# Optimization experiments

Measured on AMD Instinct MI355X. Metric: run time of the kernel, lower is better.

The kernel has to match this reference:

```python
import jax, jax.numpy as jnp
import numpy as np

B, S, D = 2, 2048, 768
H = 12
HD = D // H  # 64
SCALE = HD ** -0.5


def setup_inputs() -> dict:
    key = jax.random.key(0)
    k1, k2, k3, k4, k5 = jax.random.split(key, 5)
    x = jax.random.normal(k1, (B, S, D), dtype=jnp.float32)
    w_qkv = jax.random.normal(k2, (D, 3 * D), dtype=jnp.float32) * (D ** -0.5)
    b_qkv = jax.random.normal(k3, (3 * D,), dtype=jnp.float32) * 0.02
    w_proj = jax.random.normal(k4, (D, D), dtype=jnp.float32) * (D ** -0.5)
    b_proj = jax.random.normal(k5, (D,), dtype=jnp.float32) * 0.02
    return {"x": x, "w_qkv": w_qkv, "b_qkv": b_qkv, "w_proj": w_proj, "b_proj": b_proj}


def reference(x, w_qkv, b_qkv, w_proj, b_proj):
    b, s, d = x.shape
    # QKV projection: (B,S,3D) -> (3,B,H,S,HD)
    qkv = x @ w_qkv + b_qkv
    qkv = qkv.reshape(b, s, 3, H, HD).transpose(2, 0, 3, 1, 4)
    q, k, v = qkv[0], qkv[1], qkv[2]
    q = q * SCALE
    # full NxN attention scores, as in the original module
    attn = jnp.einsum("bhqd,bhkd->bhqk", q, k)
    attn = jax.nn.softmax(attn, axis=-1)
    out = jnp.einsum("bhqk,bhkd->bhqd", attn, v)  # (B,H,S,HD)
    out = out.transpose(0, 2, 1, 3).reshape(b, s, d)
    return out @ w_proj + b_proj
```

## Files before the change

kernel.cpp:

```cpp
#include <hip/hip_runtime.h>
#include <hip/hip_bf16.h>

#define B_ 2
#define S_ 2048
#define D_ 768
#define H_ 12
#define HD_ 64
#define EXP2C_ 0.1803368801111244f

typedef __attribute__((ext_vector_type(8))) short bf16x8;
typedef __attribute__((ext_vector_type(8))) unsigned short u16x8;
typedef __attribute__((ext_vector_type(4))) float f32x4;
typedef __attribute__((ext_vector_type(4))) unsigned int u32x4;

static __device__ __forceinline__ unsigned short f2bf(float x) {
    union { float f; unsigned u; } v; v.f = x;
    unsigned r = (v.u + 0x7FFFu + ((v.u >> 16) & 1u)) >> 16;
    return (unsigned short)r;
}
static __device__ __forceinline__ float bf2f(unsigned short h) {
    union { unsigned u; float f; } v; v.u = ((unsigned)h) << 16;
    return v.f;
}
static __device__ __forceinline__ float fexp2(float x) { return __builtin_exp2f(x); }

static __device__ __forceinline__ unsigned pk_bf16(float a, float b) {
    __hip_bfloat162 pk = __float22bfloat162_rn(make_float2(a, b));
    union { __hip_bfloat162 h; unsigned u; } v; v.h = pk;
    return v.u;
}

static __device__ __forceinline__ f32x4 mfma32(bf16x8 a, bf16x8 b, f32x4 c) {
    return __builtin_amdgcn_mfma_f32_16x16x32_bf16(a, b, c, 0, 0, 0);
}

typedef __attribute__((address_space(3))) unsigned int lds_u32;
typedef __attribute__((address_space(1))) const unsigned int glb_u32;
static __device__ __forceinline__ void glds16(const unsigned short* g, unsigned short* l) {
    __builtin_amdgcn_global_load_lds((glb_u32*)g, (lds_u32*)l, 16, 0, 0);
}

#define PREP_CONV_ 1536
#define PREP_TQKV_ 1728
#define PREP_TPRJ_ 576
__global__ __launch_bounds__(256) void prep_kernel(
    const float* __restrict__ x,      unsigned short* __restrict__ x16,
    const float* __restrict__ w_qkv,  unsigned short* __restrict__ wqkvT,
    const float* __restrict__ w_proj, unsigned short* __restrict__ wprojT)
{
    __shared__ float tile[32][33];
    const int bid = blockIdx.x, t = threadIdx.x;
    if (bid < PREP_CONV_) {
        const int i = (bid * 256 + t) * 8;
        float4 a0 = *(const float4*)(x + i);
        float4 a1 = *(const float4*)(x + i + 4);
        u16x8 s;
        s[0] = f2bf(a0.x); s[1] = f2bf(a0.y); s[2] = f2bf(a0.z); s[3] = f2bf(a0.w);
        s[4] = f2bf(a1.x); s[5] = f2bf(a1.y); s[6] = f2bf(a1.z); s[7] = f2bf(a1.w);
        *(u16x8*)(x16 + i) = s;
        return;
    }
    const float* w; unsigned short* wT; int N, bb;
    if (bid < PREP_CONV_ + PREP_TQKV_) { w = w_qkv; wT = wqkvT; N = 3 * D_; bb = bid - PREP_CONV_; }
    else                               { w = w_proj; wT = wprojT; N = D_;   bb = bid - PREP_CONV_ - PREP_TQKV_; }
    const int K = D_;
    const int nt = N / 32;
    const int n0 = (bb % nt) * 32, k0 = (bb / nt) * 32;
    const int tx = t & 31, ty = t >> 5;
#pragma unroll
    for (int i = 0; i < 4; i++)
        tile[ty + i * 8][tx] = w[(size_t)(k0 + ty + i * 8) * N + n0 + tx];
    __syncthreads();
#pragma unroll
    for (int i = 0; i < 4; i++)
        wT[(size_t)(n0 + ty + i * 8) * K + k0 + tx] = f2bf(tile[tx][ty + i * 8]);
}

template <int BM, int BN, bool OUT_F32>
__global__ __launch_bounds__(256) void gemm_bt_kernel(
    const unsigned short* __restrict__ A,
    const unsigned short* __restrict__ Bt,
    const float* __restrict__ bias,
    void* __restrict__ Cp,
    int M, int N, int K)
{
    constexpr int BK = 64;
    __shared__ __align__(16) unsigned short As[BM][BK];
    __shared__ __align__(16) unsigned short Bs[BN][BK];
    constexpr int MI = BM / 32, NJ = BN / 32;
    constexpr int ACH = BM * BK / 8;
    constexpr int BCH = BN * BK / 8;

    const int t = threadIdx.x;
    const int w = t >> 6, lane = t & 63, quad = lane >> 4, l16 = lane & 15;
    const int n0 = blockIdx.x * BN, m0 = blockIdx.y * BM;
    const int mw = (w & 1) * (BM / 2), nw = (w >> 1) * (BN / 2);

    const f32x4 z = {0.f, 0.f, 0.f, 0.f};
    f32x4 acc[MI][NJ];
#pragma unroll
    for (int i = 0; i < MI; i++)
#pragma unroll
        for (int j = 0; j < NJ; j++) acc[i][j] = z;

    for (int kk = 0; kk < K; kk += BK) {
#pragma unroll
        for (int it = 0; it < ACH / 256; it++) {
            const int c = t + it * 256;
            const int row = c >> 3, gs = (c & 7) ^ (row & 7);
            glds16(A + (size_t)(m0 + row) * K + kk + gs * 8, &As[0][0] + c * 8);
        }
#pragma unroll
        for (int it = 0; it < BCH / 256; it++) {
            const int c = t + it * 256;
            const int row = c >> 3, gs = (c & 7) ^ (row & 7);
            glds16(Bt + (size_t)(n0 + row) * K + kk + gs * 8, &Bs[0][0] + c * 8);
        }
        __syncthreads();

#pragma unroll
        for (int k2 = 0; k2 < 2; k2++) {
            bf16x8 a[MI], b[NJ];
#pragma unroll
            for (int i = 0; i < MI; i++) {
                const int row = mw + i * 16 + l16;
                const int p = (quad + k2 * 4) ^ (row & 7);
                a[i] = *(const bf16x8*)(&As[row][p * 8]);
            }
#pragma unroll
            for (int j = 0; j < NJ; j++) {
                const int row = nw + j * 16 + l16;
                const int p = (quad + k2 * 4) ^ (row & 7);
                b[j] = *(const bf16x8*)(&Bs[row][p * 8]);
            }
#pragma unroll
            for (int i = 0; i < MI; i++)
#pragma unroll
                for (int j = 0; j < NJ; j++)
                    acc[i][j] = mfma32(a[i], b[j], acc[i][j]);
        }
        __syncthreads();
    }

#pragma unroll
    for (int j = 0; j < NJ; j++) {
        const int col = n0 + nw + j * 16 + l16;
        const float bv = bias[col];
#pragma unroll
        for (int i = 0; i < MI; i++) {
#pragma unroll
            for (int r = 0; r < 4; r++) {
                const int row = m0 + mw + i * 16 + quad * 4 + r;
                const float v = acc[i][j][r] + bv;
                if (OUT_F32) ((float*)Cp)[(size_t)row * N + col] = v;
                else         ((unsigned short*)Cp)[(size_t)row * N + col] = f2bf(v);
            }
        }
    }
}

__global__ __launch_bounds__(256) void repack_v_kernel(
    const unsigned short* __restrict__ qkv,
    unsigned short* __restrict__ vt)
{
    __shared__ unsigned short T[64][65];
    const int t = threadIdx.x;
    const int bh = blockIdx.x, st = blockIdx.y;
    const int b = bh / H_, h = bh % H_;
    const unsigned short* src =
        qkv + (size_t)(b * S_ + st * 64) * (3 * D_) + 2 * D_ + h * HD_;

#pragma unroll
    for (int it = 0; it < 2; it++) {
        const int c = t + it * 256, sr = c >> 3, g = c & 7;
        u16x8 v = *(const u16x8*)(src + (size_t)sr * (3 * D_) + g * 8);
#pragma unroll
        for (int j = 0; j < 8; j++) T[sr][g * 8 + j] = v[j];
    }
    __syncthreads();
#pragma unroll
    for (int it = 0; it < 2; it++) {
        const int c = t + it * 256, hd = c >> 3, g = c & 7;
        u16x8 v;
#pragma unroll
        for (int j = 0; j < 8; j++) v[j] = T[g * 8 + j][hd];
        *(u16x8*)(vt + (size_t)(bh * HD_ + hd) * S_ + st * 64 + g * 8) = v;
    }
}

__global__ __launch_bounds__(256) void attn_kernel(
    const unsigned short* __restrict__ qkv,
    const unsigned short* __restrict__ vt,
    float* __restrict__ o_p0,
    float* __restrict__ o_p1,
    float* __restrict__ l_p)
{
    __shared__ __align__(16) unsigned short Ks[2][64][64];
    __shared__ __align__(16) unsigned short Vs[2][64][64];

    const int t = threadIdx.x;
    const int w = t >> 6, lane = t & 63, quad = lane >> 4, l16 = lane & 15;
    const int h8 = l16 & 7;
    const int qt = blockIdx.x, bh = blockIdx.y, ks = blockIdx.z;
    const int b = bh / H_, h = bh % H_;
    const int ld = 3 * D_;

    const unsigned short* qbase =
        qkv + (size_t)(b * S_ + qt * 64 + 16 * w + l16) * ld + h * HD_;
    u16x8 qr0 = *(const u16x8*)(qbase + quad * 8);
    u16x8 qr1 = *(const u16x8*)(qbase + 32 + quad * 8);
    bf16x8 qf0, qf1;
#pragma unroll
    for (int j = 0; j < 8; j++) {
        qf0[j] = (short)f2bf(bf2f(qr0[j]) * EXP2C_);
        qf1[j] = (short)f2bf(bf2f(qr1[j]) * EXP2C_);
    }

    bf16x8 ones;
#pragma unroll
    for (int j = 0; j < 8; j++) ones[j] = (short)0x3F80;

    const unsigned short* kbase =
        qkv + (size_t)(b * S_ + ks * 1024) * ld + D_ + h * HD_;
    const unsigned short* vbase = vt + (size_t)bh * HD_ * S_;

    const int c0 = t, c1 = t + 256;
    const int row0 = c0 >> 3, row1 = c1 >> 3;
    const int kg0 = (c0 & 7) ^ ((row0 & 3) | (((row0 >> 3) & 1) << 2));
    const int kg1 = (c1 & 7) ^ ((row1 & 3) | (((row1 >> 3) & 1) << 2));
    const int vg0 = (c0 & 7) ^ (row0 & 7);
    const int vg1 = (c1 & 7) ^ (row1 & 7);
    const unsigned short* kp0 = kbase + (size_t)row0 * ld + kg0 * 8;
    const unsigned short* kp1 = kbase + (size_t)row1 * ld + kg1 * 8;
    const unsigned short* vp0 = vbase + (size_t)row0 * S_ + ks * 1024 + vg0 * 8;
    const unsigned short* vp1 = vbase + (size_t)row1 * S_ + ks * 1024 + vg1 * 8;
    const size_t KSTEP = (size_t)64 * ld;

    const f32x4 z = {0.f, 0.f, 0.f, 0.f};
    f32x4 o_acc[4] = {z, z, z, z};
    f32x4 l_acc = z;

    glds16(kp0, &Ks[0][0][0] + c0 * 8);
    glds16(kp1, &Ks[0][0][0] + c1 * 8);
    glds16(vp0, &Vs[0][0][0] + c0 * 8);
    glds16(vp1, &Vs[0][0][0] + c1 * 8);
    kp0 += KSTEP; kp1 += KSTEP; vp0 += 64; vp1 += 64;
    __syncthreads();

    const int NT = 1024 / 64;
    for (int kt = 0; kt < NT; kt++) {
        const int buf = kt & 1;

        if (kt + 1 < NT) {
            unsigned short* kd = &Ks[buf ^ 1][0][0];
            unsigned short* vd = &Vs[buf ^ 1][0][0];
            glds16(kp0, kd + c0 * 8);
            glds16(kp1, kd + c1 * 8);
            glds16(vp0, vd + c0 * 8);
            glds16(vp1, vd + c1 * 8);
            kp0 += KSTEP; kp1 += KSTEP; vp0 += 64; vp1 += 64;
        }

        f32x4 s_acc[4] = {z, z, z, z};
        __builtin_amdgcn_s_setprio(1);
#pragma unroll
        for (int nt = 0; nt < 4; nt++) {
            const int rowp = ((nt >> 1) << 5) + ((l16 >> 2) << 3) + ((nt & 1) << 2) + (l16 & 3);
            const int skr = (rowp & 3) | (((rowp >> 3) & 1) << 2);
            const unsigned short* kr = &Ks[buf][rowp][0];
            bf16x8 k0 = *(const bf16x8*)(kr + (quad ^ skr) * 8);
            bf16x8 k1 = *(const bf16x8*)(kr + ((quad ^ skr) ^ 4) * 8);
            s_acc[nt] = mfma32(k0, qf0, s_acc[nt]);
            s_acc[nt] = mfma32(k1, qf1, s_acc[nt]);
        }
        __builtin_amdgcn_s_setprio(0);

        bf16x8 vr0[4], vr1[4];
#pragma unroll
        for (int nt = 0; nt < 4; nt++) {
            const int row = nt * 16 + l16;
            vr0[nt] = *(const bf16x8*)(&Vs[buf][row][(quad ^ h8) * 8]);
            vr1[nt] = *(const bf16x8*)(&Vs[buf][row][((quad ^ h8) ^ 4) * 8]);
        }

        f32x4 pr[4];
#pragma unroll
        for (int nt = 0; nt < 4; nt++) {
#pragma unroll
            for (int r = 0; r < 4; r++) pr[nt][r] = fexp2(s_acc[nt][r]);
        }
        union { u32x4 u; bf16x8 h; } ca, cb;
        ca.u[0] = pk_bf16(pr[0][0], pr[0][1]);
        ca.u[1] = pk_bf16(pr[0][2], pr[0][3]);
        ca.u[2] = pk_bf16(pr[1][0], pr[1][1]);
        ca.u[3] = pk_bf16(pr[1][2], pr[1][3]);
        cb.u[0] = pk_bf16(pr[2][0], pr[2][1]);
        cb.u[1] = pk_bf16(pr[2][2], pr[2][3]);
        cb.u[2] = pk_bf16(pr[3][0], pr[3][1]);
        cb.u[3] = pk_bf16(pr[3][2], pr[3][3]);
        const bf16x8 pa0 = ca.h, pa1 = cb.h;

        __builtin_amdgcn_s_setprio(1);
        l_acc = mfma32(pa0, ones, l_acc);
        l_acc = mfma32(pa1, ones, l_acc);
#pragma unroll
        for (int nt = 0; nt < 4; nt++) {
            o_acc[nt] = mfma32(pa0, vr0[nt], o_acc[nt]);
            o_acc[nt] = mfma32(pa1, vr1[nt], o_acc[nt]);
        }
        __builtin_amdgcn_s_setprio(0);

        __syncthreads();
    }

    float* op = ks ? o_p1 : o_p0;
    float* lp2 = l_p + (size_t)ks * (B_ * S_ * H_);
#pragma unroll
    for (int r = 0; r < 4; r++) {
        const int row = b * S_ + qt * 64 + 16 * w + quad * 4 + r;
        float* ob = op + (size_t)row * D_ + h * HD_;
#pragma unroll
        for (int nt = 0; nt < 4; nt++)
            ob[nt * 16 + l16] = o_acc[nt][r];
        if (l16 == 0) lp2[(size_t)row * H_ + h] = l_acc[r];
    }
}

__global__ __launch_bounds__(256) void combine_kernel(
    const float* __restrict__ o_p0,
    const float* __restrict__ o_p1,
    const float* __restrict__ l_p,
    unsigned short* __restrict__ o)
{
    const int i = (blockIdx.x * 256 + threadIdx.x) * 8;
    const int row = i / D_, col = i - row * D_, h = col >> 6;
    const float l0 = l_p[(size_t)row * H_ + h];
    const float l1 = l_p[(size_t)(B_ * S_ * H_) + row * H_ + h];
    const float inv = 1.f / (l0 + l1);
    float4 a0 = *(const float4*)(o_p0 + i);
    float4 a1 = *(const float4*)(o_p0 + i + 4);
    float4 b0 = *(const float4*)(o_p1 + i);
    float4 b1 = *(const float4*)(o_p1 + i + 4);
    u16x8 s;
    s[0] = f2bf((a0.x + b0.x) * inv); s[1] = f2bf((a0.y + b0.y) * inv);
    s[2] = f2bf((a0.z + b0.z) * inv); s[3] = f2bf((a0.w + b0.w) * inv);
    s[4] = f2bf((a1.x + b1.x) * inv); s[5] = f2bf((a1.y + b1.y) * inv);
    s[6] = f2bf((a1.z + b1.z) * inv); s[7] = f2bf((a1.w + b1.w) * inv);
    *(u16x8*)(o + i) = s;
}

extern "C" void kernel_launch(void* const* d_in, const int* in_sizes, int n_in,
                              void* d_out, int out_size, void* d_ws, size_t ws_size,
                              hipStream_t stream) {
    const float* x      = (const float*)d_in[0];
    const float* w_qkv  = (const float*)d_in[1];
    const float* b_qkv  = (const float*)d_in[2];
    const float* w_proj = (const float*)d_in[3];
    const float* b_proj = (const float*)d_in[4];
    float* out = (float*)d_out;

    unsigned short* qkv    = (unsigned short*)d_ws;
    unsigned short* vtb    = qkv    + (size_t)(B_ * S_) * (3 * D_);
    unsigned short* o_x16  = vtb    + (size_t)(B_ * H_) * HD_ * S_;
    unsigned short* wqkvT  = o_x16  + (size_t)(B_ * S_) * D_;
    unsigned short* wprojT = wqkvT  + (size_t)D_ * (3 * D_);
    float* o_p1 = (float*)(wprojT + (size_t)D_ * D_);
    float* l_p  = o_p1 + (size_t)(B_ * S_) * D_;
    float* o_p0 = out;

    dim3 blk(256);
    prep_kernel<<<dim3(PREP_CONV_ + PREP_TQKV_ + PREP_TPRJ_), blk, 0, stream>>>(
        x, o_x16, w_qkv, wqkvT, w_proj, wprojT);
    gemm_bt_kernel<128, 96, false><<<dim3((3 * D_) / 96, (B_ * S_) / 128), blk, 0, stream>>>(
        o_x16, wqkvT, b_qkv, qkv, B_ * S_, 3 * D_, D_);
    repack_v_kernel<<<dim3(B_ * H_, S_ / 64), blk, 0, stream>>>(qkv, vtb);
    attn_kernel<<<dim3(S_ / 64, B_ * H_, 2), blk, 0, stream>>>(qkv, vtb, o_p0, o_p1, l_p);
    combine_kernel<<<dim3((B_ * S_) * D_ / (256 * 8)), blk, 0, stream>>>(
        o_p0, o_p1, l_p, o_x16);
    gemm_bt_kernel<64, 64, true><<<dim3(D_ / 64, (B_ * S_) / 64), blk, 0, stream>>>(
        o_x16, wprojT, b_proj, out, B_ * S_, D_, D_);
}
```

Before: 171.2 us.

## Fuse V transpose into QKV GEMM epilogue and remap attention grid per XCD

The QKV GEMM epilogue now writes the V columns directly in transposed per-head layout, so the separate repack_v kernel and its extra read and write of V are no longer needed. The attention launch becomes a 1D grid whose block index is remapped so that all query tiles of one (head, split) group land on the same XCD, aiming for better L2 reuse of K/V. The s_setprio hints around the MFMA sections are also removed. The transposed V store writes 8-byte chunks with a large stride, which may coalesce poorly, and the block remapping assumes a fixed count of 8 XCDs.

```diff
diff --git a/kernel.cpp b/kernel.cpp
--- a/kernel.cpp
+++ b/kernel.cpp
@@ -76,12 +76,13 @@
         wT[(size_t)(n0 + ty + i * 8) * K + k0 + tx] = f2bf(tile[tx][ty + i * 8]);
 }
 
-template <int BM, int BN, bool OUT_F32>
+template <int BM, int BN, bool OUT_F32, bool VSPLIT>
 __global__ __launch_bounds__(256) void gemm_bt_kernel(
     const unsigned short* __restrict__ A,
     const unsigned short* __restrict__ Bt,
     const float* __restrict__ bias,
     void* __restrict__ Cp,
+    unsigned short* __restrict__ vt,
     int M, int N, int K)
 {
     constexpr int BK = 64;
@@ -142,6 +143,28 @@
         __syncthreads();
     }
 
+    if (VSPLIT && n0 >= 2 * D_) {
+#pragma unroll
+        for (int j = 0; j < NJ; j++) {
+            const int gcol = n0 + nw + j * 16 + l16;
+            const int col = gcol - 2 * D_;
+            const int hh = col >> 6, hd = col & 63;
+            const float bv = bias[gcol];
+#pragma unroll
+            for (int i = 0; i < MI; i++) {
+                const int row = m0 + mw + i * 16 + quad * 4;
+                const int bb = row >> 11, ss = row & 2047;
+                unsigned long long pkv = 0;
+#pragma unroll
+                for (int r = 0; r < 4; r++)
+                    pkv |= (unsigned long long)f2bf(acc[i][j][r] + bv) << (16 * r);
+                *(unsigned long long*)(vt +
+                    ((size_t)(bb * H_ + hh) * HD_ + hd) * S_ + ss) = pkv;
+            }
+        }
+        return;
+    }
+
 #pragma unroll
     for (int j = 0; j < NJ; j++) {
         const int col = n0 + nw + j * 16 + l16;
@@ -156,35 +179,6 @@
                 else         ((unsigned short*)Cp)[(size_t)row * N + col] = f2bf(v);
             }
         }
-    }
-}
-
-__global__ __launch_bounds__(256) void repack_v_kernel(
-    const unsigned short* __restrict__ qkv,
-    unsigned short* __restrict__ vt)
-{
-    __shared__ unsigned short T[64][65];
-    const int t = threadIdx.x;
-    const int bh = blockIdx.x, st = blockIdx.y;
-    const int b = bh / H_, h = bh % H_;
-    const unsigned short* src =
-        qkv + (size_t)(b * S_ + st * 64) * (3 * D_) + 2 * D_ + h * HD_;
-
-#pragma unroll
-    for (int it = 0; it < 2; it++) {
-        const int c = t + it * 256, sr = c >> 3, g = c & 7;
-        u16x8 v = *(const u16x8*)(src + (size_t)sr * (3 * D_) + g * 8);
-#pragma unroll
-        for (int j = 0; j < 8; j++) T[sr][g * 8 + j] = v[j];
-    }
-    __syncthreads();
-#pragma unroll
-    for (int it = 0; it < 2; it++) {
-        const int c = t + it * 256, hd = c >> 3, g = c & 7;
-        u16x8 v;
-#pragma unroll
-        for (int j = 0; j < 8; j++) v[j] = T[g * 8 + j][hd];
-        *(u16x8*)(vt + (size_t)(bh * HD_ + hd) * S_ + st * 64 + g * 8) = v;
     }
 }
 
@@ -201,7 +195,11 @@
     const int t = threadIdx.x;
     const int w = t >> 6, lane = t & 63, quad = lane >> 4, l16 = lane & 15;
     const int h8 = l16 & 7;
-    const int qt = blockIdx.x, bh = blockIdx.y, ks = blockIdx.z;
+    const int id = blockIdx.x;
+    const int xcd = id & 7, ix = id >> 3;
+    const int grp = xcd * 6 + (ix >> 5);
+    const int qt = ix & 31;
+    const int bh = grp >> 1, ks = grp & 1;
     const int b = bh / H_, h = bh % H_;
     const int ld = 3 * D_;
 
@@ -262,7 +260,6 @@
         }
 
         f32x4 s_acc[4] = {z, z, z, z};
-        __builtin_amdgcn_s_setprio(1);
 #pragma unroll
         for (int nt = 0; nt < 4; nt++) {
             const int rowp = ((nt >> 1) << 5) + ((l16 >> 2) << 3) + ((nt & 1) << 2) + (l16 & 3);
@@ -273,7 +270,6 @@
             s_acc[nt] = mfma32(k0, qf0, s_acc[nt]);
             s_acc[nt] = mfma32(k1, qf1, s_acc[nt]);
         }
-        __builtin_amdgcn_s_setprio(0);
 
         bf16x8 vr0[4], vr1[4];
 #pragma unroll
@@ -300,15 +296,14 @@
         cb.u[3] = pk_bf16(pr[3][2], pr[3][3]);
         const bf16x8 pa0 = ca.h, pa1 = cb.h;
 
-        __builtin_amdgcn_s_setprio(1);
         l_acc = mfma32(pa0, ones, l_acc);
         l_acc = mfma32(pa1, ones, l_acc);
+
 #pragma unroll
         for (int nt = 0; nt < 4; nt++) {
             o_acc[nt] = mfma32(pa0, vr0[nt], o_acc[nt]);
             o_acc[nt] = mfma32(pa1, vr1[nt], o_acc[nt]);
         }
-        __builtin_amdgcn_s_setprio(0);
 
         __syncthreads();
     }
@@ -371,12 +366,12 @@
     dim3 blk(256);
     prep_kernel<<<dim3(PREP_CONV_ + PREP_TQKV_ + PREP_TPRJ_), blk, 0, stream>>>(
         x, o_x16, w_qkv, wqkvT, w_proj, wprojT);
-    gemm_bt_kernel<128, 96, false><<<dim3((3 * D_) / 96, (B_ * S_) / 128), blk, 0, stream>>>(
-        o_x16, wqkvT, b_qkv, qkv, B_ * S_, 3 * D_, D_);
-    repack_v_kernel<<<dim3(B_ * H_, S_ / 64), blk, 0, stream>>>(qkv, vtb);
-    attn_kernel<<<dim3(S_ / 64, B_ * H_, 2), blk, 0, stream>>>(qkv, vtb, o_p0, o_p1, l_p);
+    gemm_bt_kernel<128, 96, false, true><<<dim3((3 * D_) / 96, (B_ * S_) / 128), blk, 0, stream>>>(
+        o_x16, wqkvT, b_qkv, qkv, vtb, B_ * S_, 3 * D_, D_);
+    attn_kernel<<<dim3((S_ / 64) * (B_ * H_) * 2), blk, 0, stream>>>(
+        qkv, vtb, o_p0, o_p1, l_p);
     combine_kernel<<<dim3((B_ * S_) * D_ / (256 * 8)), blk, 0, stream>>>(
         o_p0, o_p1, l_p, o_x16);
-    gemm_bt_kernel<64, 64, true><<<dim3(D_ / 64, (B_ * S_) / 64), blk, 0, stream>>>(
-        o_x16, wprojT, b_proj, out, B_ * S_, D_, D_);
-}
+    gemm_bt_kernel<64, 64, true, false><<<dim3(D_ / 64, (B_ * S_) / 64), blk, 0, stream>>>(
+        o_x16, wprojT, b_proj, out, nullptr, B_ * S_, D_, D_);
+}
```

Measured after the change: 165.5 us. 3.4% less time.
